# Kernel optimization log

Measured on AMD Instinct MI355X. Metric: run time of the kernel, lower is better.

The kernel has to match this reference:

```python
import jax, jax.numpy as jnp
import numpy as np

LN_EPS = 1e-5
L2_EPS = 1e-12
SCALE = 8.0

def setup_inputs() -> dict:
    key = jax.random.key(0)
    k0, k1, k2 = jax.random.split(key, 3)
    b, c, H, W = 16, 256, 64, 64
    heads, dim_head = 8, 32
    dim_inner = heads * dim_head  # 256
    x = jax.random.normal(k0, (b, c, H, W), dtype=jnp.float32)
    ln_gamma = jnp.ones((c,), jnp.float32)
    ln_beta = jnp.zeros((c,), jnp.float32)
    W_qkv = jax.random.normal(k1, (c, 3 * dim_inner), dtype=jnp.float32) * 0.02
    temperature = jnp.ones((heads,), jnp.float32)
    W_out = jax.random.normal(k2, (dim_inner, c), dtype=jnp.float32) * 0.02
    b_out = jnp.zeros((c,), jnp.float32)
    return {"x": x, "ln_gamma": ln_gamma, "ln_beta": ln_beta, "W_qkv": W_qkv,
            "temperature": temperature, "W_out": W_out, "b_out": b_out, "heads": heads}

def _l2norm(t):
    # F.normalize(t, dim=-1): divide by clamped L2 norm along last axis
    n = jnp.sqrt(jnp.sum(t * t, axis=-1, keepdims=True))
    return t / jnp.maximum(n, L2_EPS)

def reference(x, ln_gamma, ln_beta, W_qkv, temperature, W_out, b_out, heads):
    b, c, H, W = x.shape
    n = H * W
    dim_head = W_qkv.shape[1] // (3 * heads)
    # b c h w -> b (h w) c
    t = jnp.transpose(x, (0, 2, 3, 1)).reshape(b, n, c)
    # LayerNorm over channel dim (affine)
    mu = jnp.mean(t, axis=-1, keepdims=True)
    var = jnp.mean(jnp.square(t - mu), axis=-1, keepdims=True)
    t = (t - mu) * jax.lax.rsqrt(var + LN_EPS) * ln_gamma + ln_beta
    # qkv projection; split last dim as (qkv, heads, dim_head) -> (3, b, h, d, n)
    qkv = (t @ W_qkv).reshape(b, n, 3, heads, dim_head)
    qkv = jnp.transpose(qkv, (2, 0, 3, 4, 1))
    q, k, v = qkv[0], qkv[1], qkv[2]
    q = _l2norm(q) * jnp.exp(temperature)[None, :, None, None]
    k = _l2norm(k)
    # cross-covariance attention over channel dim: sim is [b, h, d, d]
    sim = jnp.einsum('bhin,bhjn->bhij', q, k) * SCALE
    attn = jax.nn.softmax(sim, axis=-1)
    out = jnp.einsum('bhij,bhjn->bhin', attn, v)  # [b, h, d, n]
    # b h d n -> b n (h d)
    out = jnp.transpose(out, (0, 3, 1, 2)).reshape(b, n, heads * dim_head)
    out = out @ W_out + b_out
    # b (h w) c -> b c h w
    return jnp.transpose(out.reshape(b, H, W, c), (0, 3, 1, 2))
```

## Files before the change

### kernel.cpp

```cpp
#include <hip/hip_runtime.h>

typedef unsigned short u16;
typedef __bf16 bf16x8 __attribute__((ext_vector_type(8)));
typedef float f32x4 __attribute__((ext_vector_type(4)));

#define MFMA(a, b, c) __builtin_amdgcn_mfma_f32_16x16x32_bf16((a), (b), (c), 0, 0, 0)

__device__ __forceinline__ u16 f2bf(float f) {
    unsigned u = __float_as_uint(f);
    unsigned r = (u + 0x7fffu + ((u >> 16) & 1u)) >> 16;
    return (u16)r;
}
__device__ __forceinline__ float bf2f(u16 h) { return __uint_as_float(((unsigned)h) << 16); }

typedef unsigned int u32_g __attribute__((address_space(1)));
typedef unsigned int u32_l __attribute__((address_space(3)));
__device__ __forceinline__ void gload16(const void* g, void* l) {
    __builtin_amdgcn_global_load_lds((const u32_g*)g, (u32_l*)l, 16, 0, 0);
}


__global__ __launch_bounds__(1024) void k_lngram(const float* __restrict__ x,
                                                 const float* __restrict__ gamma,
                                                 const float* __restrict__ beta,
                                                 u16* __restrict__ xlnT, float* __restrict__ Gp) {
    __shared__ __align__(16) unsigned smem[256 * 64];
    float* sf = (float*)smem;
    int bid = blockIdx.x;
    int b = bid >> 4, ch = bid & 15;
    int t = threadIdx.x;
    int np = t & 63, cg = t >> 6;
    int lane = t & 63, l15 = lane & 15, quad = lane >> 4;
    int w = t >> 6;
    int mr2 = (w & 7) * 2, nf0 = (w >> 3) * 8;
    f32x4 acc[2][8];
    {
        f32x4 z = {0.f, 0.f, 0.f, 0.f};
        for (int fm = 0; fm < 2; fm++)
            for (int j = 0; j < 8; j++) acc[fm][j] = z;
    }
    for (int sc = 0; sc < 2; sc++) {
        int nb = ch * 256 + sc * 128;
        const float* xp = x + ((size_t)(b * 256 + cg * 16)) * 4096 + nb + np * 2;
        float2 v[16];
        float s0 = 0.f, s1 = 0.f, s20 = 0.f, s21 = 0.f;
#pragma unroll
        for (int i = 0; i < 16; i++) {
            float2 f = *(const float2*)(xp + (size_t)i * 4096);
            v[i] = f;
            s0 += f.x; s20 += f.x * f.x;
            s1 += f.y; s21 += f.y * f.y;
        }
        if (sc) __syncthreads();
        sf[cg * 128 + 2 * np] = s0;
        sf[cg * 128 + 2 * np + 1] = s1;
        sf[2048 + cg * 128 + 2 * np] = s20;
        sf[2048 + cg * 128 + 2 * np + 1] = s21;
        __syncthreads();
        if (t < 128) {
            float s = 0.f, s2 = 0.f;
#pragma unroll
            for (int g = 0; g < 16; g++) { s += sf[g * 128 + t]; s2 += sf[2048 + g * 128 + t]; }
            float m = s * (1.f / 256.f);
            float var = s2 * (1.f / 256.f) - m * m;
            sf[4096 + t] = m;
            sf[4224 + t] = rsqrtf(var + 1e-5f);
        }
        __syncthreads();
        float m0 = sf[4096 + 2 * np], r0 = sf[4224 + 2 * np];
        float m1 = sf[4096 + 2 * np + 1], r1 = sf[4224 + 2 * np + 1];
        __syncthreads();
        u16 hA[16], hB[16];
#pragma unroll
        for (int i = 0; i < 16; i++) {
            int c = cg * 16 + i;
            float g = gamma[c], e = beta[c];
            float a = (v[i].x - m0) * r0 * g + e;
            float bv = (v[i].y - m1) * r1 * g + e;
            u16 ha = f2bf(a), hb = f2bf(bv);
            hA[i] = ha; hB[i] = hb;
            int dw = c * 64 + ((((np >> 2) ^ (c & 15)) << 2) | (np & 3));
            smem[dw] = (unsigned)ha | ((unsigned)hb << 16);
        }
        {
            u16* dst0 = xlnT + ((size_t)(b * 4096 + nb + 2 * np)) * 256 + cg * 16;
            uint4 qa, qb;
            qa.x = (unsigned)hA[0] | ((unsigned)hA[1] << 16);
            qa.y = (unsigned)hA[2] | ((unsigned)hA[3] << 16);
            qa.z = (unsigned)hA[4] | ((unsigned)hA[5] << 16);
            qa.w = (unsigned)hA[6] | ((unsigned)hA[7] << 16);
            qb.x = (unsigned)hA[8] | ((unsigned)hA[9] << 16);
            qb.y = (unsigned)hA[10] | ((unsigned)hA[11] << 16);
            qb.z = (unsigned)hA[12] | ((unsigned)hA[13] << 16);
            qb.w = (unsigned)hA[14] | ((unsigned)hA[15] << 16);
            *(uint4*)dst0 = qa;
            *(uint4*)(dst0 + 8) = qb;
            u16* dst1 = dst0 + 256;
            qa.x = (unsigned)hB[0] | ((unsigned)hB[1] << 16);
            qa.y = (unsigned)hB[2] | ((unsigned)hB[3] << 16);
            qa.z = (unsigned)hB[4] | ((unsigned)hB[5] << 16);
            qa.w = (unsigned)hB[6] | ((unsigned)hB[7] << 16);
            qb.x = (unsigned)hB[8] | ((unsigned)hB[9] << 16);
            qb.y = (unsigned)hB[10] | ((unsigned)hB[11] << 16);
            qb.z = (unsigned)hB[12] | ((unsigned)hB[13] << 16);
            qb.w = (unsigned)hB[14] | ((unsigned)hB[15] << 16);
            *(uint4*)dst1 = qa;
            *(uint4*)(dst1 + 8) = qb;
        }
        __syncthreads();
#pragma unroll
        for (int ks = 0; ks < 4; ks++) {
            int ca0 = (mr2 * 16 + l15);
            int ca1 = ((mr2 + 1) * 16 + l15);
            bf16x8 a0 = *(const bf16x8*)&smem[ca0 * 64 + (((ks * 4 + quad) ^ (ca0 & 15)) << 2)];
            bf16x8 a1 = *(const bf16x8*)&smem[ca1 * 64 + (((ks * 4 + quad) ^ (ca1 & 15)) << 2)];
#pragma unroll
            for (int j = 0; j < 8; j++) {
                int cb = ((nf0 + j) * 16 + l15);
                bf16x8 bb = *(const bf16x8*)&smem[cb * 64 + (((ks * 4 + quad) ^ (cb & 15)) << 2)];
                acc[0][j] = MFMA(a0, bb, acc[0][j]);
                acc[1][j] = MFMA(a1, bb, acc[1][j]);
            }
        }
    }
    float* gp = Gp + (size_t)(b * 16 + ch) * 65536;
    for (int fm = 0; fm < 2; fm++)
        for (int j = 0; j < 8; j++)
            for (int r = 0; r < 4; r++) {
                int row = (mr2 + fm) * 16 + quad * 4 + r;
                int col = (nf0 + j) * 16 + l15;
                gp[row * 256 + col] = acc[fm][j][r];
            }
}

__global__ __launch_bounds__(256) void k_prep(const float* __restrict__ Wqkv,
                                              const float* __restrict__ Wout,
                                              u16* __restrict__ WqkvT, u16* __restrict__ WvTn,
                                              u16* __restrict__ WoutT) {
    int i = blockIdx.x * 256 + threadIdx.x;
    if (i < 512 * 256) { int o = i >> 8, c = i & 255; WqkvT[i] = f2bf(Wqkv[c * 768 + o]); }
    if (i < 256 * 256) {
        int e = i >> 8, o = i & 255;
        WvTn[i] = f2bf(Wqkv[e * 768 + 512 + o]);
        WoutT[i] = f2bf(Wout[o * 256 + e]);
    }
}

__global__ __launch_bounds__(256) void k_g2b(const float* __restrict__ Gp,
                                             u16* __restrict__ Ghi, u16* __restrict__ Glo) {
    int g = blockIdx.x * 256 + threadIdx.x;
    int b = g >> 14, e = g & 16383;
    const float4* p = (const float4*)Gp + (size_t)(b * 16) * 16384 + e;
    float4 s = p[0];
#pragma unroll
    for (int j = 1; j < 16; j++) {
        float4 v = p[(size_t)j * 16384];
        s.x += v.x; s.y += v.y; s.z += v.z; s.w += v.w;
    }
    u16 h0 = f2bf(s.x), h1 = f2bf(s.y), h2 = f2bf(s.z), h3 = f2bf(s.w);
    u16 l0 = f2bf(s.x - bf2f(h0)), l1 = f2bf(s.y - bf2f(h1));
    u16 l2 = f2bf(s.z - bf2f(h2)), l3 = f2bf(s.w - bf2f(h3));
    uint2 ph; ph.x = (unsigned)h0 | ((unsigned)h1 << 16); ph.y = (unsigned)h2 | ((unsigned)h3 << 16);
    uint2 pl; pl.x = (unsigned)l0 | ((unsigned)l1 << 16); pl.y = (unsigned)l2 | ((unsigned)l3 << 16);
    *(uint2*)(Ghi + (size_t)g * 4) = ph;
    *(uint2*)(Glo + (size_t)g * 4) = pl;
}

__global__ __launch_bounds__(256) void k_sq(const u16* __restrict__ A,
                                            const u16* __restrict__ Ghi, const u16* __restrict__ Glo,
                                            u16* __restrict__ Shi, u16* __restrict__ Slo) {
    __shared__ __align__(16) u16 aT[128 * 32];
    __shared__ __align__(16) u16 bT[128 * 32];
    int bid = blockIdx.x;
    int b = bid >> 3;
    int r2 = bid & 7;
    int mbase = (r2 >> 1) * 128, nbase = (r2 & 1) * 128;
    int t = threadIdx.x, w = t >> 6, lane = t & 63, l15 = lane & 15, quad = lane >> 4;
    int srow = lane >> 2;
    int g8 = (((lane & 3) ^ ((lane >> 3) & 3)) << 3);
    const u16* gA = A + (size_t)(mbase + w * 32 + srow) * 256 + g8;
    const u16* gBh = Ghi + (size_t)b * 65536 + (size_t)(nbase + w * 32 + srow) * 256 + g8;
    const u16* gBl = Glo + (size_t)b * 65536 + (size_t)(nbase + w * 32 + srow) * 256 + g8;
    u16* lA = aT + w * 1024;
    u16* lB = bT + w * 1024;
    int cOff = ((quad ^ ((l15 >> 1) & 3)) << 3);
    f32x4 acc[2][8];
    f32x4 z = {0.f, 0.f, 0.f, 0.f};
    for (int fm = 0; fm < 2; fm++)
        for (int fn = 0; fn < 8; fn++) acc[fm][fn] = z;
    for (int kt = 0; kt < 16; kt++) {
        int kb = (kt & 7) * 32;
        const u16* gB = (kt < 8) ? gBh : gBl;
        if (kt) __syncthreads();
        gload16(gA + kb, lA);
        gload16(gA + 16 * 256 + kb, lA + 512);
        gload16(gB + kb, lB);
        gload16(gB + 16 * 256 + kb, lB + 512);
        __syncthreads();
        bf16x8 af0 = *(const bf16x8*)&aT[(w * 32 + l15) * 32 + cOff];
        bf16x8 af1 = *(const bf16x8*)&aT[(w * 32 + 16 + l15) * 32 + cOff];
        for (int fn = 0; fn < 8; fn++) {
            bf16x8 bfr = *(const bf16x8*)&bT[(fn * 16 + l15) * 32 + cOff];
            acc[0][fn] = MFMA(af0, bfr, acc[0][fn]);
            acc[1][fn] = MFMA(af1, bfr, acc[1][fn]);
        }
    }
    for (int fm = 0; fm < 2; fm++)
        for (int fn = 0; fn < 8; fn++)
            for (int r = 0; r < 4; r++) {
                int row = mbase + w * 32 + fm * 16 + quad * 4 + r;
                int col = nbase + fn * 16 + l15;
                float v = acc[fm][fn][r];
                u16 hi = f2bf(v);
                Shi[((size_t)b * 512 + row) * 256 + col] = hi;
                Slo[((size_t)b * 512 + row) * 256 + col] = f2bf(v - bf2f(hi));
            }
}

__global__ __launch_bounds__(256) void k_gemm(const u16* __restrict__ A, size_t aStrB,
                                              const u16* __restrict__ Bb, size_t bStrB,
                                              int mtiles, int ntiles,
                                              u16* __restrict__ o16, float* __restrict__ o32,
                                              const float* __restrict__ bias,
                                              size_t oStrB, int oRstr, int mode) {
    __shared__ __align__(16) u16 aT[128 * 32];
    __shared__ __align__(16) u16 bT[128 * 32];
    int bid = blockIdx.x;
    int per_b = mtiles * ntiles;
    int b = bid / per_b;
    int r2 = bid % per_b;
    int mbase = (r2 / ntiles) * 128, nbase = (r2 % ntiles) * 128;
    int t = threadIdx.x, w = t >> 6, lane = t & 63, l15 = lane & 15, quad = lane >> 4;
    const u16* Ap = A + (size_t)b * aStrB;
    const u16* Bp = Bb + (size_t)b * bStrB;
    int srow = lane >> 2;
    int g8 = (((lane & 3) ^ ((lane >> 3) & 3)) << 3);
    const u16* gA = Ap + (size_t)(mbase + w * 32 + srow) * 256 + g8;
    const u16* gB = Bp + (size_t)(nbase + w * 32 + srow) * 256 + g8;
    u16* lA = aT + w * 1024;
    u16* lB = bT + w * 1024;
    int cOff = ((quad ^ ((l15 >> 1) & 3)) << 3);
    f32x4 acc[2][8];
    f32x4 z = {0.f, 0.f, 0.f, 0.f};
    for (int fm = 0; fm < 2; fm++)
        for (int fn = 0; fn < 8; fn++) acc[fm][fn] = z;
    for (int kt = 0; kt < 8; kt++) {
        int kb = kt * 32;
        if (kt) __syncthreads();
        gload16(gA + kb, lA);
        gload16(gA + 16 * 256 + kb, lA + 512);
        gload16(gB + kb, lB);
        gload16(gB + 16 * 256 + kb, lB + 512);
        __syncthreads();
        bf16x8 af0 = *(const bf16x8*)&aT[(w * 32 + l15) * 32 + cOff];
        bf16x8 af1 = *(const bf16x8*)&aT[(w * 32 + 16 + l15) * 32 + cOff];
        for (int fn = 0; fn < 8; fn++) {
            bf16x8 bfr = *(const bf16x8*)&bT[(fn * 16 + l15) * 32 + cOff];
            acc[0][fn] = MFMA(af0, bfr, acc[0][fn]);
            acc[1][fn] = MFMA(af1, bfr, acc[1][fn]);
        }
    }
    if (mode == 0) {
        for (int fm = 0; fm < 2; fm++)
            for (int fn = 0; fn < 8; fn++)
                for (int r = 0; r < 4; r++) {
                    int row = mbase + w * 32 + fm * 16 + quad * 4 + r;
                    int col = nbase + fn * 16 + l15;
                    o16[(size_t)b * oStrB + (size_t)row * oRstr + col] = f2bf(acc[fm][fn][r]);
                }
    } else {
        for (int fm = 0; fm < 2; fm++)
            for (int fn = 0; fn < 8; fn++)
                for (int r = 0; r < 4; r++) {
                    int row = mbase + w * 32 + fm * 16 + quad * 4 + r;
                    int col = nbase + fn * 16 + l15;
                    o32[(size_t)b * oStrB + (size_t)row * oRstr + col] = acc[fm][fn][r] + bias[row];
                }
    }
}

__global__ __launch_bounds__(256) void k_out(const u16* __restrict__ F, const u16* __restrict__ xlnT,
                                             const float* __restrict__ bias, float* __restrict__ out) {
    __shared__ __align__(16) u16 aT[256 * 32];
    __shared__ __align__(16) u16 bT[128 * 32];
    int bid = blockIdx.x;
    int b = bid >> 5, nt = bid & 31;
    int nbase = nt * 128;
    int t = threadIdx.x, w = t >> 6, lane = t & 63, l15 = lane & 15, quad = lane >> 4;
    int srow = lane >> 2;
    int g8 = (((lane & 3) ^ ((lane >> 3) & 3)) << 3);
    const u16* gA = F + (size_t)b * 65536 + (size_t)(w * 64 + srow) * 256 + g8;
    const u16* gB = xlnT + (size_t)b * 4096 * 256 + (size_t)(nbase + w * 32 + srow) * 256 + g8;
    u16* lA = aT + w * 2048;
    u16* lB = bT + w * 1024;
    int cOff = ((quad ^ ((l15 >> 1) & 3)) << 3);
    f32x4 acc[4][8];
    f32x4 z = {0.f, 0.f, 0.f, 0.f};
    for (int fm = 0; fm < 4; fm++)
        for (int fn = 0; fn < 8; fn++) acc[fm][fn] = z;
    for (int kt = 0; kt < 8; kt++) {
        int kb = kt * 32;
        if (kt) __syncthreads();
        gload16(gA + kb, lA);
        gload16(gA + 16 * 256 + kb, lA + 512);
        gload16(gA + 32 * 256 + kb, lA + 1024);
        gload16(gA + 48 * 256 + kb, lA + 1536);
        gload16(gB + kb, lB);
        gload16(gB + 16 * 256 + kb, lB + 512);
        __syncthreads();
        bf16x8 af[4];
#pragma unroll
        for (int fm = 0; fm < 4; fm++)
            af[fm] = *(const bf16x8*)&aT[(w * 64 + fm * 16 + l15) * 32 + cOff];
        for (int fn = 0; fn < 8; fn++) {
            bf16x8 bfr = *(const bf16x8*)&bT[(fn * 16 + l15) * 32 + cOff];
#pragma unroll
            for (int fm = 0; fm < 4; fm++) acc[fm][fn] = MFMA(af[fm], bfr, acc[fm][fn]);
        }
    }
    for (int fm = 0; fm < 4; fm++)
        for (int fn = 0; fn < 8; fn++)
            for (int r = 0; r < 4; r++) {
                int row = w * 64 + fm * 16 + quad * 4 + r;
                int col = nbase + fn * 16 + l15;
                out[((size_t)b * 256 + row) * 4096 + col] = acc[fm][fn][r] + bias[row];
            }
}

__global__ __launch_bounds__(256) void k_attn(const u16* __restrict__ Shi,
                                              const u16* __restrict__ Slo,
                                              const u16* __restrict__ WqkvT,
                                              const u16* __restrict__ WoutT,
                                              const float* __restrict__ temp,
                                              u16* __restrict__ M_all) {
    int bh = blockIdx.x;
    int b = bh >> 3, h = bh & 7;
    __shared__ u16 sqh[32 * 264], sql[32 * 264], skh[32 * 264], wq[32 * 264], wk[32 * 264];
    __shared__ u16 wo[256 * 40];
    __shared__ u16 attnT[32 * 40];
    __shared__ float simS[32 * 33];
    __shared__ float redn[4 * 64];
    __shared__ float scq[32], sck[32];
    int t = threadIdx.x, w = t >> 6, lane = t & 63, l15 = lane & 15, quad = lane >> 4;
    {
        int r = t >> 3, cc0 = (t & 7) * 32;
        const u16* gqh = Shi + ((size_t)(b * 512) + h * 32 + r) * 256 + cc0;
        const u16* gql = Slo + ((size_t)(b * 512) + h * 32 + r) * 256 + cc0;
        const u16* gkh = Shi + ((size_t)(b * 512) + 256 + h * 32 + r) * 256 + cc0;
        const u16* gwq = WqkvT + (size_t)(h * 32 + r) * 256 + cc0;
        const u16* gwk = WqkvT + (size_t)(256 + h * 32 + r) * 256 + cc0;
#pragma unroll
        for (int k = 0; k < 4; k++) {
            *(uint4*)&sqh[r * 264 + cc0 + k * 8] = *(const uint4*)(gqh + k * 8);
            *(uint4*)&sql[r * 264 + cc0 + k * 8] = *(const uint4*)(gql + k * 8);
            *(uint4*)&skh[r * 264 + cc0 + k * 8] = *(const uint4*)(gkh + k * 8);
            *(uint4*)&wq[r * 264 + cc0 + k * 8] = *(const uint4*)(gwq + k * 8);
            *(uint4*)&wk[r * 264 + cc0 + k * 8] = *(const uint4*)(gwk + k * 8);
        }
        const u16* gwo = WoutT + (size_t)t * 256 + h * 32;
#pragma unroll
        for (int k = 0; k < 4; k++) *(uint4*)&wo[t * 40 + k * 8] = *(const uint4*)(gwo + k * 8);
    }
    __syncthreads();
    {
        int rn = t & 63, cc = t >> 6;
        int e0 = cc * 64;
        float s = 0.f;
        if (rn < 32) {
            const u16* ph = &sqh[rn * 264];
            const u16* pl = &sql[rn * 264];
            const u16* pb = &wq[rn * 264];
            for (int e = 0; e < 64; e++)
                s += (bf2f(ph[e0 + e]) + bf2f(pl[e0 + e])) * bf2f(pb[e0 + e]);
        } else {
            const u16* ph = &skh[(rn - 32) * 264];
            const u16* pb = &wk[(rn - 32) * 264];
            for (int e = 0; e < 64; e++)
                s += bf2f(ph[e0 + e]) * bf2f(pb[e0 + e]);
        }
        redn[cc * 64 + rn] = s;
    }
    {
        int iq = w >> 1, jq = w & 1;
        f32x4 acc = {0.f, 0.f, 0.f, 0.f};
        for (int s8 = 0; s8 < 8; s8++) {
            bf16x8 a = *(const bf16x8*)&sqh[(iq * 16 + l15) * 264 + s8 * 32 + quad * 8];
            bf16x8 bb = *(const bf16x8*)&wk[(jq * 16 + l15) * 264 + s8 * 32 + quad * 8];
            acc = MFMA(a, bb, acc);
        }
        for (int s8 = 0; s8 < 8; s8++) {
            bf16x8 a = *(const bf16x8*)&sql[(iq * 16 + l15) * 264 + s8 * 32 + quad * 8];
            bf16x8 bb = *(const bf16x8*)&wk[(jq * 16 + l15) * 264 + s8 * 32 + quad * 8];
            acc = MFMA(a, bb, acc);
        }
        for (int r = 0; r < 4; r++)
            simS[(iq * 16 + quad * 4 + r) * 33 + jq * 16 + l15] = acc[r];
    }
    __syncthreads();
    if (t < 32)
        scq[t] = expf(temp[h]) * 8.0f /
                 fmaxf(sqrtf(redn[t] + redn[64 + t] + redn[128 + t] + redn[192 + t]), 1e-12f);
    else if (t < 64) {
        int d = t - 32;
        sck[d] = 1.0f / fmaxf(sqrtf(redn[32 + d] + redn[96 + d] + redn[160 + d] + redn[224 + d]), 1e-12f);
    }
    __syncthreads();
    if (t < 32) {
        float row[32];
        float m = -1e30f, sqv = scq[t];
#pragma unroll
        for (int j = 0; j < 32; j++) {
            float v = simS[t * 33 + j] * sqv * sck[j];
            row[j] = v; m = fmaxf(m, v);
        }
        float s = 0.f;
#pragma unroll
        for (int j = 0; j < 32; j++) { float p = expf(row[j] - m); row[j] = p; s += p; }
        float inv = 1.f / s;
#pragma unroll
        for (int j = 0; j < 32; j++) attnT[j * 40 + t] = f2bf(row[j] * inv);
    }
    __syncthreads();
    {
        f32x4 z = {0.f, 0.f, 0.f, 0.f};
        for (int mf = 0; mf < 4; mf++) {
            bf16x8 a = *(const bf16x8*)&wo[((w * 4 + mf) * 16 + l15) * 40 + quad * 8];
            for (int nf = 0; nf < 2; nf++) {
                bf16x8 bb = *(const bf16x8*)&attnT[(nf * 16 + l15) * 40 + quad * 8];
                f32x4 d = MFMA(a, bb, z);
                for (int r = 0; r < 4; r++) {
                    int c = (w * 4 + mf) * 16 + quad * 4 + r;
                    M_all[((size_t)(b * 256) + c) * 256 + h * 32 + nf * 16 + l15] = f2bf(d[r]);
                }
            }
        }
    }
}

extern "C" void kernel_launch(void* const* d_in, const int* in_sizes, int n_in,
                              void* d_out, int out_size, void* d_ws, size_t ws_size,
                              hipStream_t stream) {
    const float* x     = (const float*)d_in[0];
    const float* gamma = (const float*)d_in[1];
    const float* beta  = (const float*)d_in[2];
    const float* Wqkv  = (const float*)d_in[3];
    const float* temp  = (const float*)d_in[4];
    const float* Wout  = (const float*)d_in[5];
    const float* bout  = (const float*)d_in[6];
    float* out = (float*)d_out;

    char* ws = (char*)d_ws;
    size_t off = 0;
    auto alloc = [&](size_t nbytes) -> void* {
        void* p = ws + off;
        off = (off + nbytes + 255) & ~(size_t)255;
        return p;
    };
    u16* xlnT   = (u16*)alloc((size_t)16 * 4096 * 256 * 2);
    u16* WqkvT  = (u16*)alloc((size_t)512 * 256 * 2);
    u16* WvTn   = (u16*)alloc((size_t)256 * 256 * 2);
    u16* WoutT  = (u16*)alloc((size_t)256 * 256 * 2);
    float* Gp   = (float*)alloc((size_t)256 * 65536 * 4);
    u16* Gbh    = (u16*)alloc((size_t)16 * 65536 * 2);
    u16* Gbl    = (u16*)alloc((size_t)16 * 65536 * 2);
    u16* Sqh    = (u16*)alloc((size_t)16 * 512 * 256 * 2);
    u16* Sql    = (u16*)alloc((size_t)16 * 512 * 256 * 2);
    u16* M_all  = (u16*)alloc((size_t)16 * 256 * 256 * 2);
    u16* F      = (u16*)alloc((size_t)16 * 256 * 256 * 2);
    (void)ws_size; (void)in_sizes; (void)n_in; (void)out_size;

    hipLaunchKernelGGL(k_prep, dim3(1024), dim3(256), 0, stream, Wqkv, Wout, WqkvT, WvTn, WoutT);
    hipLaunchKernelGGL(k_lngram, dim3(256), dim3(1024), 0, stream, x, gamma, beta, xlnT, Gp);
    hipLaunchKernelGGL(k_g2b, dim3(1024), dim3(256), 0, stream, Gp, Gbh, Gbl);
    hipLaunchKernelGGL(k_sq, dim3(128), dim3(256), 0, stream, WqkvT, Gbh, Gbl, Sqh, Sql);
    hipLaunchKernelGGL(k_attn, dim3(128), dim3(256), 0, stream, Sqh, Sql, WqkvT, WoutT, temp, M_all);
    hipLaunchKernelGGL(k_gemm, dim3(64), dim3(256), 0, stream,
                       M_all, (size_t)65536, WvTn, (size_t)0, 2, 2,
                       F, (float*)nullptr, (const float*)nullptr,
                       (size_t)65536, 256, 0);
    hipLaunchKernelGGL(k_out, dim3(512), dim3(256), 0, stream, F, xlnT, bout, out);
}
```

Before: 255.5 us.

## Split Gram row-halves across blocks, prefetch x chunks, fuse prep into reduce

```diff
diff --git a/kernel.cpp b/kernel.cpp
--- a/kernel.cpp
+++ b/kernel.cpp
@@ -27,63 +27,68 @@
     __shared__ __align__(16) unsigned smem[256 * 64];
     float* sf = (float*)smem;
     int bid = blockIdx.x;
-    int b = bid >> 4, ch = bid & 15;
+    int s = bid >> 7;
+    int bc = bid & 127;
+    int b = bc >> 3, ch = bc & 7;
     int t = threadIdx.x;
-    int np = t & 63, cg = t >> 6;
+    int np = t & 15, cgl = (t >> 4) & 15, g = t >> 8;
     int lane = t & 63, l15 = lane & 15, quad = lane >> 4;
     int w = t >> 6;
-    int mr2 = (w & 7) * 2, nf0 = (w >> 3) * 8;
-    f32x4 acc[2][8];
+    int mr = w & 7, nh = w >> 3;
+    int c0 = cgl * 16;
+    int nl0 = g * 32 + 2 * np;
+    int npg = g * 16 + np;
+    int slot = npg >> 2, rem = npg & 3;
+    f32x4 acc[8];
     {
         f32x4 z = {0.f, 0.f, 0.f, 0.f};
-        for (int fm = 0; fm < 2; fm++)
-            for (int j = 0; j < 8; j++) acc[fm][j] = z;
-    }
-    for (int sc = 0; sc < 2; sc++) {
-        int nb = ch * 256 + sc * 128;
-        const float* xp = x + ((size_t)(b * 256 + cg * 16)) * 4096 + nb + np * 2;
-        float2 v[16];
+        for (int j = 0; j < 8; j++) acc[j] = z;
+    }
+    const float* xp = x + ((size_t)(b * 256 + c0)) * 4096 + ch * 512 + nl0;
+    float2 v[16];
+#pragma unroll
+    for (int i = 0; i < 16; i++) v[i] = *(const float2*)(xp + (size_t)i * 4096);
+    for (int sc = 0; sc < 4; sc++) {
+        int nb = ch * 512 + sc * 128;
         float s0 = 0.f, s1 = 0.f, s20 = 0.f, s21 = 0.f;
 #pragma unroll
         for (int i = 0; i < 16; i++) {
-            float2 f = *(const float2*)(xp + (size_t)i * 4096);
-            v[i] = f;
+            float2 f = v[i];
             s0 += f.x; s20 += f.x * f.x;
             s1 += f.y; s21 += f.y * f.y;
         }
         if (sc) __syncthreads();
-        sf[cg * 128 + 2 * np] = s0;
-        sf[cg * 128 + 2 * np + 1] = s1;
-        sf[2048 + cg * 128 + 2 * np] = s20;
-        sf[2048 + cg * 128 + 2 * np + 1] = s21;
+        sf[nl0 * 17 + cgl] = s0;
+        sf[(nl0 + 1) * 17 + cgl] = s1;
+        sf[2304 + nl0 * 17 + cgl] = s20;
+        sf[2304 + (nl0 + 1) * 17 + cgl] = s21;
         __syncthreads();
         if (t < 128) {
-            float s = 0.f, s2 = 0.f;
-#pragma unroll
-            for (int g = 0; g < 16; g++) { s += sf[g * 128 + t]; s2 += sf[2048 + g * 128 + t]; }
-            float m = s * (1.f / 256.f);
-            float var = s2 * (1.f / 256.f) - m * m;
-            sf[4096 + t] = m;
-            sf[4224 + t] = rsqrtf(var + 1e-5f);
-        }
-        __syncthreads();
-        float m0 = sf[4096 + 2 * np], r0 = sf[4224 + 2 * np];
-        float m1 = sf[4096 + 2 * np + 1], r1 = sf[4224 + 2 * np + 1];
+            float a = 0.f, a2 = 0.f;
+#pragma unroll
+            for (int jj = 0; jj < 16; jj++) { a += sf[t * 17 + jj]; a2 += sf[2304 + t * 17 + jj]; }
+            float m = a * (1.f / 256.f);
+            float var = a2 * (1.f / 256.f) - m * m;
+            sf[4608 + t] = m;
+            sf[4800 + t] = rsqrtf(var + 1e-5f);
+        }
+        __syncthreads();
+        float m0 = sf[4608 + nl0], r0 = sf[4800 + nl0];
+        float m1 = sf[4608 + nl0 + 1], r1 = sf[4800 + nl0 + 1];
         __syncthreads();
         u16 hA[16], hB[16];
 #pragma unroll
         for (int i = 0; i < 16; i++) {
-            int c = cg * 16 + i;
-            float g = gamma[c], e = beta[c];
-            float a = (v[i].x - m0) * r0 * g + e;
-            float bv = (v[i].y - m1) * r1 * g + e;
+            int c = c0 + i;
+            float ga = gamma[c], e = beta[c];
+            float a = (v[i].x - m0) * r0 * ga + e;
+            float bv = (v[i].y - m1) * r1 * ga + e;
             u16 ha = f2bf(a), hb = f2bf(bv);
             hA[i] = ha; hB[i] = hb;
-            int dw = c * 64 + ((((np >> 2) ^ (c & 15)) << 2) | (np & 3));
-            smem[dw] = (unsigned)ha | ((unsigned)hb << 16);
-        }
-        {
-            u16* dst0 = xlnT + ((size_t)(b * 4096 + nb + 2 * np)) * 256 + cg * 16;
+            smem[c * 64 + (((slot ^ (c & 15)) << 2) | rem)] = (unsigned)ha | ((unsigned)hb << 16);
+        }
+        if ((cgl >> 3) == s) {
+            u16* dst0 = xlnT + ((size_t)(b * 4096 + nb + nl0)) * 256 + c0;
             uint4 qa, qb;
             qa.x = (unsigned)hA[0] | ((unsigned)hA[1] << 16);
             qa.y = (unsigned)hA[2] | ((unsigned)hA[3] << 16);
@@ -108,32 +113,32 @@
             *(uint4*)(dst1 + 8) = qb;
         }
         __syncthreads();
+        if (sc < 3) {
+            const float* nxp = xp + (sc + 1) * 128;
+#pragma unroll
+            for (int i = 0; i < 16; i++) v[i] = *(const float2*)(nxp + (size_t)i * 4096);
+        }
+        int ca = s * 128 + mr * 16 + l15;
 #pragma unroll
         for (int ks = 0; ks < 4; ks++) {
-            int ca0 = (mr2 * 16 + l15);
-            int ca1 = ((mr2 + 1) * 16 + l15);
-            bf16x8 a0 = *(const bf16x8*)&smem[ca0 * 64 + (((ks * 4 + quad) ^ (ca0 & 15)) << 2)];
-            bf16x8 a1 = *(const bf16x8*)&smem[ca1 * 64 + (((ks * 4 + quad) ^ (ca1 & 15)) << 2)];
+            bf16x8 af = *(const bf16x8*)&smem[ca * 64 + (((ks * 4 + quad) ^ (ca & 15)) << 2)];
 #pragma unroll
             for (int j = 0; j < 8; j++) {
-                int cb = ((nf0 + j) * 16 + l15);
+                int cb = nh * 128 + j * 16 + l15;
                 bf16x8 bb = *(const bf16x8*)&smem[cb * 64 + (((ks * 4 + quad) ^ (cb & 15)) << 2)];
-                acc[0][j] = MFMA(a0, bb, acc[0][j]);
-                acc[1][j] = MFMA(a1, bb, acc[1][j]);
+                acc[j] = MFMA(af, bb, acc[j]);
             }
         }
     }
-    float* gp = Gp + (size_t)(b * 16 + ch) * 65536;
-    for (int fm = 0; fm < 2; fm++)
-        for (int j = 0; j < 8; j++)
-            for (int r = 0; r < 4; r++) {
-                int row = (mr2 + fm) * 16 + quad * 4 + r;
-                int col = (nf0 + j) * 16 + l15;
-                gp[row * 256 + col] = acc[fm][j][r];
-            }
-}
-
-__global__ __launch_bounds__(256) void k_prep(const float* __restrict__ Wqkv,
+    float* gp = Gp + (size_t)bid * 32768;
+    for (int j = 0; j < 8; j++)
+        for (int r = 0; r < 4; r++)
+            gp[(mr * 16 + quad * 4 + r) * 256 + nh * 128 + j * 16 + l15] = acc[j][r];
+}
+
+__global__ __launch_bounds__(256) void k_g2bp(const float* __restrict__ Gp,
+                                              u16* __restrict__ Ghi, u16* __restrict__ Glo,
+                                              const float* __restrict__ Wqkv,
                                               const float* __restrict__ Wout,
                                               u16* __restrict__ WqkvT, u16* __restrict__ WvTn,
                                               u16* __restrict__ WoutT) {
@@ -144,26 +149,23 @@
         WvTn[i] = f2bf(Wqkv[e * 768 + 512 + o]);
         WoutT[i] = f2bf(Wout[o * 256 + e]);
     }
-}
-
-__global__ __launch_bounds__(256) void k_g2b(const float* __restrict__ Gp,
-                                             u16* __restrict__ Ghi, u16* __restrict__ Glo) {
-    int g = blockIdx.x * 256 + threadIdx.x;
-    int b = g >> 14, e = g & 16383;
-    const float4* p = (const float4*)Gp + (size_t)(b * 16) * 16384 + e;
-    float4 s = p[0];
-#pragma unroll
-    for (int j = 1; j < 16; j++) {
-        float4 v = p[(size_t)j * 16384];
-        s.x += v.x; s.y += v.y; s.z += v.z; s.w += v.w;
-    }
-    u16 h0 = f2bf(s.x), h1 = f2bf(s.y), h2 = f2bf(s.z), h3 = f2bf(s.w);
-    u16 l0 = f2bf(s.x - bf2f(h0)), l1 = f2bf(s.y - bf2f(h1));
-    u16 l2 = f2bf(s.z - bf2f(h2)), l3 = f2bf(s.w - bf2f(h3));
+    int b = i >> 14, e = i & 16383;
+    int row = e >> 6, col4 = e & 63;
+    int slab = row >> 7, rl = row & 127;
+    const float4* p = (const float4*)(Gp + ((size_t)(slab * 128 + b * 8)) * 32768 + rl * 256 + col4 * 4);
+    float4 sv = p[0];
+#pragma unroll
+    for (int jc = 1; jc < 8; jc++) {
+        float4 vv = p[(size_t)jc * 8192];
+        sv.x += vv.x; sv.y += vv.y; sv.z += vv.z; sv.w += vv.w;
+    }
+    u16 h0 = f2bf(sv.x), h1 = f2bf(sv.y), h2 = f2bf(sv.z), h3 = f2bf(sv.w);
+    u16 l0 = f2bf(sv.x - bf2f(h0)), l1 = f2bf(sv.y - bf2f(h1));
+    u16 l2 = f2bf(sv.z - bf2f(h2)), l3 = f2bf(sv.w - bf2f(h3));
     uint2 ph; ph.x = (unsigned)h0 | ((unsigned)h1 << 16); ph.y = (unsigned)h2 | ((unsigned)h3 << 16);
     uint2 pl; pl.x = (unsigned)l0 | ((unsigned)l1 << 16); pl.y = (unsigned)l2 | ((unsigned)l3 << 16);
-    *(uint2*)(Ghi + (size_t)g * 4) = ph;
-    *(uint2*)(Glo + (size_t)g * 4) = pl;
+    *(uint2*)(Ghi + (size_t)i * 4) = ph;
+    *(uint2*)(Glo + (size_t)i * 4) = pl;
 }
 
 __global__ __launch_bounds__(256) void k_sq(const u16* __restrict__ A,
@@ -460,7 +462,7 @@
     u16* WqkvT  = (u16*)alloc((size_t)512 * 256 * 2);
     u16* WvTn   = (u16*)alloc((size_t)256 * 256 * 2);
     u16* WoutT  = (u16*)alloc((size_t)256 * 256 * 2);
-    float* Gp   = (float*)alloc((size_t)256 * 65536 * 4);
+    float* Gp   = (float*)alloc((size_t)256 * 32768 * 4);
     u16* Gbh    = (u16*)alloc((size_t)16 * 65536 * 2);
     u16* Gbl    = (u16*)alloc((size_t)16 * 65536 * 2);
     u16* Sqh    = (u16*)alloc((size_t)16 * 512 * 256 * 2);
@@ -469,9 +471,9 @@
     u16* F      = (u16*)alloc((size_t)16 * 256 * 256 * 2);
     (void)ws_size; (void)in_sizes; (void)n_in; (void)out_size;
 
-    hipLaunchKernelGGL(k_prep, dim3(1024), dim3(256), 0, stream, Wqkv, Wout, WqkvT, WvTn, WoutT);
     hipLaunchKernelGGL(k_lngram, dim3(256), dim3(1024), 0, stream, x, gamma, beta, xlnT, Gp);
-    hipLaunchKernelGGL(k_g2b, dim3(1024), dim3(256), 0, stream, Gp, Gbh, Gbl);
+    hipLaunchKernelGGL(k_g2bp, dim3(1024), dim3(256), 0, stream, Gp, Gbh, Gbl,
+                       Wqkv, Wout, WqkvT, WvTn, WoutT);
     hipLaunchKernelGGL(k_sq, dim3(128), dim3(256), 0, stream, WqkvT, Gbh, Gbl, Sqh, Sql);
     hipLaunchKernelGGL(k_attn, dim3(128), dim3(256), 0, stream, Sqh, Sql, WqkvT, WoutT, temp, M_all);
     hipLaunchKernelGGL(k_gemm, dim3(64), dim3(256), 0, stream,
```

New measurement: 242.0 us. -5.3%, faster.
